# Optimization experiments

Measured on AMD Instinct MI355X. Metric: run time of the kernel, lower is better.

## Reference

```python
import jax, jax.numpy as jnp
import numpy as np
from jax import lax

FEAT_STRIDE = 16
RATIOS = (0.5, 1.0, 2.0)
SCALES = (8.0, 16.0, 32.0)
N_ANCHOR = len(RATIOS) * len(SCALES)  # 9
PRE_NMS = 6000     # ProposalCreator test-mode n_pre_nms
POST_NMS = 300     # test-mode n_post_nms
NMS_THRESH = 0.7
MIN_SIZE = 16.0


def _anchor_base():
    base = 16.0
    py = px = base / 2.0
    r = np.asarray(RATIOS, np.float64)
    s = np.asarray(SCALES, np.float64)
    h = (base * s[None, :] * np.sqrt(r[:, None])).reshape(-1)
    w = (base * s[None, :] * np.sqrt(1.0 / r[:, None])).reshape(-1)
    return np.stack([py - h / 2, px - w / 2, py + h / 2, px + w / 2], axis=1).astype(np.float32)  # [9,4] (y1,x1,y2,x2)


def _enumerate_anchors(H, W):
    base = _anchor_base()
    sy = np.arange(H, dtype=np.float32) * FEAT_STRIDE
    sx = np.arange(W, dtype=np.float32) * FEAT_STRIDE
    yy, xx = np.meshgrid(sy, sx, indexing='ij')
    shift = np.stack([yy, xx, yy, xx], axis=-1).reshape(-1, 1, 4)  # [H*W,1,4]
    return jnp.asarray((shift + base[None]).reshape(-1, 4))  # [H*W*9, 4]


def _loc2bbox(anchors, loc):
    h = anchors[:, 2] - anchors[:, 0]
    w = anchors[:, 3] - anchors[:, 1]
    cy = anchors[:, 0] + 0.5 * h
    cx = anchors[:, 1] + 0.5 * w
    dy, dx, dh, dw = loc[:, 0], loc[:, 1], loc[:, 2], loc[:, 3]
    ny, nx = dy * h + cy, dx * w + cx
    nh, nw = jnp.exp(dh) * h, jnp.exp(dw) * w
    return jnp.stack([ny - 0.5 * nh, nx - 0.5 * nw, ny + 0.5 * nh, nx + 0.5 * nw], axis=1)


def _iou_one(box, boxes):
    ty1 = jnp.maximum(box[0], boxes[:, 0])
    tx1 = jnp.maximum(box[1], boxes[:, 1])
    ty2 = jnp.minimum(box[2], boxes[:, 2])
    tx2 = jnp.minimum(box[3], boxes[:, 3])
    inter = jnp.clip(ty2 - ty1, 0.0) * jnp.clip(tx2 - tx1, 0.0)
    a1 = (box[2] - box[0]) * (box[3] - box[1])
    a2 = (boxes[:, 2] - boxes[:, 0]) * (boxes[:, 3] - boxes[:, 1])
    return inter / jnp.maximum(a1 + a2 - inter, 1e-9)


def _nms_keep(boxes, valid):
    # boxes are sorted by descending score; greedy suppression, fixed shapes
    n = boxes.shape[0]
    idxs = jnp.arange(n)
    def body(i, keep):
        iou = _iou_one(boxes[i], boxes)
        sup = (iou > NMS_THRESH) & (idxs > i)
        return jnp.where(keep[i], keep & ~sup, keep)
    return lax.fori_loop(0, n, body, valid)


def _propose_one(loc, fg, anchors, img_h, img_w, scale):
    boxes = _loc2bbox(anchors, loc)
    boxes = jnp.stack([jnp.clip(boxes[:, 0], 0.0, img_h), jnp.clip(boxes[:, 1], 0.0, img_w),
                       jnp.clip(boxes[:, 2], 0.0, img_h), jnp.clip(boxes[:, 3], 0.0, img_w)], axis=1)
    min_sz = MIN_SIZE * scale
    hs = boxes[:, 2] - boxes[:, 0]
    ws = boxes[:, 3] - boxes[:, 1]
    ok = (hs >= min_sz) & (ws >= min_sz)
    sc = jnp.where(ok, fg, -jnp.inf)
    top_sc, top_idx = lax.top_k(sc, PRE_NMS)
    b = boxes[top_idx]
    keep = _nms_keep(b, jnp.isfinite(top_sc))
    # stable-compact kept boxes to the front, pad to POST_NMS with zeros
    order = jnp.argsort(jnp.where(keep, jnp.arange(PRE_NMS), PRE_NMS))
    sel = order[:POST_NMS]
    n_keep = jnp.sum(keep)
    mask = (jnp.arange(POST_NMS) < n_keep)[:, None].astype(b.dtype)
    return b[sel] * mask  # [POST_NMS, 4], zero-padded


def setup_inputs() -> dict:
    key = jax.random.key(0)
    ks = jax.random.split(key, 5)
    B, C, H, W = 16, 512, 50, 50
    x = jax.random.normal(ks[0], (B, C, H, W), jnp.float32)
    conv1_w = 0.01 * jax.random.normal(ks[1], (512, 512, 3, 3), jnp.float32)
    conv1_b = jnp.zeros((512,), jnp.float32)
    score_w = 0.01 * jax.random.normal(ks[2], (N_ANCHOR * 2, 512, 1, 1), jnp.float32)
    score_b = jnp.zeros((N_ANCHOR * 2,), jnp.float32)
    loc_w = 0.01 * jax.random.normal(ks[3], (N_ANCHOR * 4, 512, 1, 1), jnp.float32)
    loc_b = jnp.zeros((N_ANCHOR * 4,), jnp.float32)
    return {"x": x, "img_h": 800, "img_w": 800,
            "conv1_w": conv1_w, "conv1_b": conv1_b,
            "score_w": score_w, "score_b": score_b,
            "loc_w": loc_w, "loc_b": loc_b}


def reference(x, img_h, img_w, conv1_w, conv1_b, score_w, score_b, loc_w, loc_b):
    B, C, H, W = x.shape
    anchors = _enumerate_anchors(H, W)
    # Faithful to the source bug: `mid = self.conv1(x); mid = relu(x)` -> conv1 output is discarded.
    mid = jax.nn.relu(x)
    # 1x1 convs as einsum; permute(0,2,3,1) + view == bhwo layout then reshape
    locs = jnp.einsum('bchw,oc->bhwo', mid, loc_w[:, :, 0, 0]) + loc_b      # [B,H,W,4A]
    locs = locs.reshape(B, -1, 4)                                            # [B, H*W*A, 4]
    scores_raw = jnp.einsum('bchw,oc->bhwo', mid, score_w[:, :, 0, 0]) + score_b  # [B,H,W,2A]
    sm = jax.nn.softmax(scores_raw.reshape(B, H, W, N_ANCHOR, 2), axis=4)
    fg = sm[..., 1].reshape(B, -1)                                           # [B, H*W*A]
    scores = scores_raw.reshape(B, -1, 2)
    ih = jnp.float32(img_h)
    iw = jnp.float32(img_w)
    rois_b = jax.vmap(lambda l, f: _propose_one(l, f, anchors, ih, iw, 1.0))(locs, fg)  # [B,POST,4]
    rois = rois_b.reshape(-1, 4)
    roi_ix = jnp.repeat(jnp.arange(B, dtype=jnp.int32), POST_NMS)
    return locs, scores, rois, roi_ix, anchors
```

## Files before the change

kernel.cpp:

```cpp
#include <hip/hip_runtime.h>
#include <math.h>

#define NB 16
#define PP 2500
#define WWD 50
#define NANCH 22500
#define CIN 512
#define PRE 6000
#define POST 300
#define NW64 94
#define NW32 188
#define NSEG 16
#define SEG 1408
#define SEGP 2048
#define RUN 6016
#define NMST 512

#define OFF_LOCS   0
#define OFF_SCORES 1440000
#define OFF_ROIS   2160000
#define OFF_ROIIX  2179200
#define OFF_ANCH   2184000

typedef unsigned long long u64;
typedef unsigned u32;

__device__ __forceinline__ void g2l16(const float* g, float* l) {
    __builtin_amdgcn_global_load_lds(
        (const __attribute__((address_space(1))) void*)g,
        (__attribute__((address_space(3))) void*)l, 16, 0, 0);
}

__device__ inline float4 anchor_of(int r) {
    int p = r / 9, a = r - p * 9;
    int gy = p / WWD, gx = p - gy * WWD;
    int ri = a / 3, si = a - ri * 3;
    double ratio = (ri == 0) ? 0.5 : (ri == 1 ? 1.0 : 2.0);
    double scale = (si == 0) ? 8.0 : (si == 1 ? 16.0 : 32.0);
    double hh = 16.0 * scale * sqrt(ratio);
    double wd = 16.0 * scale * sqrt(1.0 / ratio);
    float by1 = (float)(8.0 - hh * 0.5);
    float bx1 = (float)(8.0 - wd * 0.5);
    float by2 = (float)(8.0 + hh * 0.5);
    float bx2 = (float)(8.0 + wd * 0.5);
    float sy = (float)gy * 16.0f, sx = (float)gx * 16.0f;
    return make_float4(sy + by1, sx + bx1, sy + by2, sx + bx2);
}

__device__ inline float4 decode_box(const float* __restrict__ lp, float4 an,
                                    float ih, float iw, bool* ok) {
    float dy = lp[0], dx = lp[1], dh = lp[2], dw = lp[3];
    float h = an.z - an.x, w = an.w - an.y;
    float cy = an.x + 0.5f * h, cx = an.y + 0.5f * w;
    float ny = dy * h + cy, nx = dx * w + cx;
    float nh = expf(dh) * h, nw = expf(dw) * w;
    float y1 = fminf(fmaxf(ny - 0.5f * nh, 0.f), ih);
    float x1 = fminf(fmaxf(nx - 0.5f * nw, 0.f), iw);
    float y2 = fminf(fmaxf(ny + 0.5f * nh, 0.f), ih);
    float x2 = fminf(fmaxf(nx + 0.5f * nw, 0.f), iw);
    *ok = ((y2 - y1) >= 16.0f) && ((x2 - x1) >= 16.0f);
    return make_float4(y1, x1, y2, x2);
}

__device__ inline float iou_f32(float4 a, float4 b) {
    float ty1 = fmaxf(a.x, b.x), tx1 = fmaxf(a.y, b.y);
    float ty2 = fminf(a.z, b.z), tx2 = fminf(a.w, b.w);
    float inter = fmaxf(ty2 - ty1, 0.f) * fmaxf(tx2 - tx1, 0.f);
    float aa = (a.z - a.x) * (a.w - a.y);
    float ab = (b.z - b.x) * (b.w - b.y);
    return inter / fmaxf(aa + ab - inter, 1e-9f);
}

__global__ __launch_bounds__(256) void k_gemm(
    const float* __restrict__ x, const float* __restrict__ lw, const float* __restrict__ lb,
    const float* __restrict__ sw, const float* __restrict__ sb, float* __restrict__ out)
{
    __shared__ __align__(16) float wsL[2][64][16];
    __shared__ __align__(16) float xsL[2][16][64];
    int bid = blockIdx.x;
    int b   = bid / 40;
    int pt  = bid % 40;
    int tid = threadIdx.x;
    int po  = tid & 63;
    int wv  = tid >> 6;
    int og  = __builtin_amdgcn_readfirstlane(wv);
    int ptbase = pt * 64;
    int p0  = ptbase + po;
    bool act0 = (p0 < PP);

    int o0  = og * 14;
    int cnt = (og == 3) ? 12 : 14;
    float bias[14];
#pragma unroll
    for (int k = 0; k < 14; ++k) {
        int o = o0 + k;
        int oc = (o < 54) ? o : 53;
        bias[k] = (oc < 36) ? lb[oc] : sb[oc - 36];
    }

    const float* xrow = x + (size_t)b * (CIN * PP);

    float acc0[14];
#pragma unroll
    for (int k = 0; k < 14; ++k) acc0[k] = 0.f;

    auto stage_async = [&](int buf, int c0) {
        {
            int fbase = og * 256 + po * 4;
            int cc = fbase >> 6;
            int xj = fbase & 63;
            int gpos = ptbase + xj;
            if (gpos > PP - 4) gpos = PP - 4;
            const float* gsrc = xrow + (size_t)(c0 + cc) * PP + gpos;
            float* ldst = &xsL[buf][0][0] + og * 256;
            g2l16(gsrc, ldst);
        }
        {
            int fl = og * 256 + po * 4;
            int o = fl >> 4;
            int c4 = fl & 15;
            const float* gw = (o < 36) ? (lw + (size_t)o * CIN + c0 + c4)
                            : (o < 54) ? (sw + (size_t)(o - 36) * CIN + c0 + c4)
                                       : (lw + c4);
            float* wdst = &wsL[buf][0][0] + og * 256;
            g2l16(gw, wdst);
        }
    };

    stage_async(0, 0);
    __syncthreads();

#pragma unroll 1
    for (int t = 0; t < 32; ++t) {
        int cur = t & 1;
        if (t + 1 < 32) stage_async(cur ^ 1, (t + 1) * 16);
#pragma unroll
        for (int g = 0; g < 4; ++g) {
            float x0[4];
#pragma unroll
            for (int u = 0; u < 4; ++u)
                x0[u] = fmaxf(xsL[cur][g * 4 + u][po], 0.f);
#pragma unroll
            for (int k = 0; k < 14; ++k) {
                float4 w4 = *reinterpret_cast<const float4*>(&wsL[cur][o0 + k][g * 4]);
                acc0[k] += x0[0] * w4.x;
                acc0[k] += x0[1] * w4.y;
                acc0[k] += x0[2] * w4.z;
                acc0[k] += x0[3] * w4.w;
            }
        }
        __syncthreads();
    }

    if (!act0) return;
#pragma unroll
    for (int k = 0; k < 14; ++k) {
        if (k < cnt) {
            int o = o0 + k;
            if (o < 36)
                out[(size_t)OFF_LOCS + ((size_t)b * PP + p0) * 36 + o] = acc0[k] + bias[k];
            else
                out[(size_t)OFF_SCORES + ((size_t)b * PP + p0) * 18 + (o - 36)] = acc0[k] + bias[k];
        }
    }
}

__global__ __launch_bounds__(1024) void k_sort1(
    const float* __restrict__ out_ro, float* __restrict__ out, u64* __restrict__ runs,
    const int* __restrict__ imh_p, const int* __restrict__ imw_p)
{
    __shared__ u64 sk[SEGP];
    int blk = blockIdx.x;
    int b = blk >> 4, s = blk & 15;
    int tid = threadIdx.x;
    int base = s * SEG;
    float ih = (float)imh_p[0], iw = (float)imw_p[0];

    for (int i = tid; i < SEGP; i += 1024) {
        int r = base + i;
        u64 key = 0ull;
        if (i < SEG && r < NANCH) {
            float4 an = anchor_of(r);
            if (b == 0) ((float4*)(out + OFF_ANCH))[r] = an;
            bool ok;
            (void)decode_box(out_ro + (size_t)OFF_LOCS + ((size_t)b * NANCH + r) * 4,
                             an, ih, iw, &ok);
            int p = r / 9, a = r - p * 9;
            const float* sp = out_ro + (size_t)OFF_SCORES + ((size_t)b * PP + p) * 18 + a * 2;
            float s0 = sp[0], s1 = sp[1];
            float mx = fmaxf(s0, s1);
            float e0 = expf(s0 - mx), e1 = expf(s1 - mx);
            float fg = e1 / (e0 + e1);
            float sc = ok ? fg : -INFINITY;
            u32 sb = __float_as_uint(sc);
            sb = (sb & 0x80000000u) ? ~sb : (sb | 0x80000000u);
            key = ((u64)sb << 32) | (u64)(u32)(NANCH - r);
        }
        sk[i] = key;
    }
    __syncthreads();
    for (int kk = 2; kk <= SEGP; kk <<= 1) {
        for (int j = kk >> 1; j > 0; j >>= 1) {
            for (int i = tid; i < SEGP; i += 1024) {
                int ij = i ^ j;
                if (ij > i) {
                    u64 va = sk[i], vb = sk[ij];
                    bool up = ((i & kk) == 0);
                    if (up ? (va < vb) : (va > vb)) { sk[i] = vb; sk[ij] = va; }
                }
            }
            __syncthreads();
        }
    }
    u64* dst = runs + (size_t)blk * SEGP;
    for (int i = tid; i < SEGP; i += 1024) dst[i] = sk[i];
}

__device__ inline int mp_search(const u64* __restrict__ A, const u64* __restrict__ B,
                                int LA, int LB, int d) {
    int lo = max(0, d - LB), hi = min(d, LA);
    while (lo < hi) {
        int mid = (lo + hi) >> 1;
        if (A[mid] > B[d - 1 - mid]) lo = mid + 1; else hi = mid;
    }
    return lo;
}

__global__ __launch_bounds__(1024) void k_merge(
    const u64* __restrict__ in, u64* __restrict__ outk,
    int runLen, int pairsPerBatch, int outLen)
{
    int blk = blockIdx.x;
    int b = blk / pairsPerBatch, m = blk - b * pairsPerBatch;
    const u64* A = in + ((size_t)b * pairsPerBatch * 2 + 2 * m) * runLen;
    const u64* B = A + runLen;
    u64* C = outk + ((size_t)b * pairsPerBatch + m) * outLen;
    int E = (outLen + 1023) >> 10;
    int d0 = threadIdx.x * E;
    if (d0 >= outLen) return;
    int cnt = min(E, outLen - d0);
    int i = mp_search(A, B, runLen, runLen, d0);
    int j = d0 - i;
    for (int e = 0; e < cnt; ++e) {
        u64 va = (i < runLen) ? A[i] : 0ull;
        u64 vb = (j < runLen) ? B[j] : 0ull;
        bool takeA = (j >= runLen) || ((i < runLen) && (va > vb));
        C[d0 + e] = takeA ? va : vb;
        if (takeA) ++i; else ++j;
    }
}

__global__ __launch_bounds__(1024) void k_merge_emit(
    const u64* __restrict__ in, const float* __restrict__ out_ro,
    float* __restrict__ topBoxes, u32* __restrict__ topValid,
    const int* __restrict__ imh_p, const int* __restrict__ imw_p)
{
    int b = blockIdx.x;
    const u64* A = in + (size_t)b * 2 * RUN;
    const u64* B = A + RUN;
    float ih = (float)imh_p[0], iw = (float)imw_p[0];
    int E = (PRE + 1023) >> 10;
    int d0 = threadIdx.x * E;
    if (d0 >= PRE) return;
    int cnt = min(E, PRE - d0);
    int i = mp_search(A, B, RUN, RUN, d0);
    int j = d0 - i;
    for (int e = 0; e < cnt; ++e) {
        u64 va = (i < RUN) ? A[i] : 0ull;
        u64 vb = (j < RUN) ? B[j] : 0ull;
        bool takeA = (j >= RUN) || ((i < RUN) && (va > vb));
        u64 key = takeA ? va : vb;
        if (takeA) ++i; else ++j;
        int d = d0 + e;
        bool valid = (key >> 63) != 0ull;
        int idx = valid ? (NANCH - (int)(key & 0xFFFFFFFFull)) : 0;
        bool ok;
        float4 an = anchor_of(idx);
        float4 bx = decode_box(out_ro + (size_t)OFF_LOCS + ((size_t)b * NANCH + idx) * 4,
                               an, ih, iw, &ok);
        ((float4*)topBoxes)[(size_t)b * PRE + d] = bx;
        topValid[(size_t)b * PRE + d] = valid ? 1u : 0u;
    }
}

__global__ __launch_bounds__(NMST) void k_nms(const float* __restrict__ topBoxes,
                                              const u32* __restrict__ topValid,
                                              float* __restrict__ out)
{
    __shared__ float4 chunkB[64];
    __shared__ float4 keptB[POST];
    __shared__ u32 sup[NW32];
    __shared__ int s_nk;
    __shared__ int s_stop;
    int b = blockIdx.x, tid = threadIdx.x;
    int wave = tid >> 6, lane = tid & 63;
    const float4* tb = (const float4*)topBoxes + (size_t)b * PRE;

    for (int i = tid; i < NW32; i += NMST) sup[i] = 0u;
    if (tid == 0) { s_nk = 0; s_stop = 0; }
    __syncthreads();
    for (int r = tid; r < PRE; r += NMST)
        if (!topValid[(size_t)b * PRE + r]) atomicOr(&sup[r >> 5], 1u << (r & 31));
    if (tid == 0) atomicOr(&sup[187], 0xFFFF0000u);
    __syncthreads();

    for (int c = 0; c < NW64; ++c) {
        int base = c * 64;
        if (tid < 64)
            chunkB[tid] = (base + tid < PRE) ? tb[base + tid]
                                             : make_float4(0.f, 0.f, 0.f, 0.f);
        int nk0 = s_nk;
        bool s = false;
        if (nk0 > 0 && base + lane < PRE) {
            float4 bj = tb[base + lane];
            for (int t = wave; t < nk0; t += 8)
                s |= iou_f32(keptB[t], bj) > 0.7f;
        }
        u64 bal = __ballot(s);
        if (lane == 0 && bal) {
            atomicOr(&sup[2 * c], (u32)bal);
            atomicOr(&sup[2 * c + 1], (u32)(bal >> 32));
        }
        __syncthreads();
        if (wave == 0) {
            u64 avail = ~(((u64)sup[2 * c + 1] << 32) | (u64)sup[2 * c]);
            float4 myB = chunkB[lane];
            int nkl = s_nk;
            while (avail && nkl < POST) {
                int i = __builtin_ctzll(avail);
                float4 bi = chunkB[i];
                if (lane == 0) keptB[nkl] = bi;
                nkl++;
                bool ss = iou_f32(bi, myB) > 0.7f;
                u64 bb = __ballot(ss);
                avail &= ~((1ull << i) | bb);
            }
            if (lane == 0) { s_nk = nkl; if (nkl >= POST) s_stop = 1; }
        }
        __syncthreads();
        if (s_stop) break;
    }

    __syncthreads();
    int nk = min(s_nk, POST);
    for (int r = tid; r < POST; r += NMST) {
        float4 v = make_float4(0.f, 0.f, 0.f, 0.f);
        if (r < nk) v = keptB[r];
        ((float4*)(out + OFF_ROIS))[(size_t)b * POST + r] = v;
        out[(size_t)OFF_ROIIX + (size_t)b * POST + r] = (float)b;
    }
}

extern "C" void kernel_launch(void* const* d_in, const int* in_sizes, int n_in,
                              void* d_out, int out_size, void* d_ws, size_t ws_size,
                              hipStream_t stream) {
    const float* x  = (const float*)d_in[0];
    const int* imh  = (const int*)d_in[1];
    const int* imw  = (const int*)d_in[2];
    const float* sw = (const float*)d_in[5];
    const float* sb = (const float*)d_in[6];
    const float* lw = (const float*)d_in[7];
    const float* lb = (const float*)d_in[8];
    float* out = (float*)d_out;
    char* wsb = (char*)d_ws;

    u64*   runs0    = (u64*)(wsb);
    u64*   runs1    = (u64*)(wsb + 4194304);
    u64*   runs2    = (u64*)(wsb + 8388608);
    u64*   runs3    = (u64*)(wsb + 11468800);
    float* topBoxes = (float*)(wsb + 13008896);
    u32*   topValid = (u32*)(wsb + 14544896);

    hipLaunchKernelGGL(k_gemm, dim3(NB * 40), dim3(256), 0, stream,
                       x, lw, lb, sw, sb, out);
    hipLaunchKernelGGL(k_sort1, dim3(NB * NSEG), dim3(1024), 0, stream,
                       out, out, runs0, imh, imw);
    hipLaunchKernelGGL(k_merge, dim3(NB * 8), dim3(1024), 0, stream,
                       runs0, runs1, SEGP, 8, 4096);
    hipLaunchKernelGGL(k_merge, dim3(NB * 4), dim3(1024), 0, stream,
                       runs1, runs2, 4096, 4, RUN);
    hipLaunchKernelGGL(k_merge, dim3(NB * 2), dim3(1024), 0, stream,
                       runs2, runs3, RUN, 2, RUN);
    hipLaunchKernelGGL(k_merge_emit, dim3(NB), dim3(1024), 0, stream,
                       runs3, out, topBoxes, topValid, imh, imw);
    hipLaunchKernelGGL(k_nms, dim3(NB), dim3(NMST), 0, stream,
                       topBoxes, topValid, out);
}
```

Baseline: 239.8 us.

## Fuse merge passes into two kernels with shared-memory intermediate runs

Replaces the four merge-path kernel launches with two. Each new kernel does two merge levels, keeping the first level's output in LDS instead of writing it to global memory. This removes two launches and two global round trips of the intermediate sorted runs. In exchange it uses 64 KB and 96 KB of shared memory per block, which cuts occupancy, and the final merge runs on only 16 blocks.

```diff
diff --git a/kernel.cpp b/kernel.cpp
--- a/kernel.cpp
+++ b/kernel.cpp
@@ -216,8 +216,7 @@
     for (int i = tid; i < SEGP; i += 1024) dst[i] = sk[i];
 }
 
-__device__ inline int mp_search(const u64* __restrict__ A, const u64* __restrict__ B,
-                                int LA, int LB, int d) {
+__device__ inline int mp_search(const u64* A, const u64* B, int LA, int LB, int d) {
     int lo = max(0, d - LB), hi = min(d, LA);
     while (lo < hi) {
         int mid = (lo + hi) >> 1;
@@ -226,48 +225,68 @@
     return lo;
 }
 
-__global__ __launch_bounds__(1024) void k_merge(
-    const u64* __restrict__ in, u64* __restrict__ outk,
-    int runLen, int pairsPerBatch, int outLen)
-{
-    int blk = blockIdx.x;
-    int b = blk / pairsPerBatch, m = blk - b * pairsPerBatch;
-    const u64* A = in + ((size_t)b * pairsPerBatch * 2 + 2 * m) * runLen;
-    const u64* B = A + runLen;
-    u64* C = outk + ((size_t)b * pairsPerBatch + m) * outLen;
-    int E = (outLen + 1023) >> 10;
-    int d0 = threadIdx.x * E;
-    if (d0 >= outLen) return;
-    int cnt = min(E, outLen - d0);
-    int i = mp_search(A, B, runLen, runLen, d0);
+__device__ inline void mp_merge_seg(const u64* A, const u64* B, int LA, int LB,
+                                    int d0, int cnt, u64* dst) {
+    int i = mp_search(A, B, LA, LB, d0);
     int j = d0 - i;
     for (int e = 0; e < cnt; ++e) {
-        u64 va = (i < runLen) ? A[i] : 0ull;
-        u64 vb = (j < runLen) ? B[j] : 0ull;
-        bool takeA = (j >= runLen) || ((i < runLen) && (va > vb));
-        C[d0 + e] = takeA ? va : vb;
+        u64 va = (i < LA) ? A[i] : 0ull;
+        u64 vb = (j < LB) ? B[j] : 0ull;
+        bool takeA = (j >= LB) || ((i < LA) && (va > vb));
+        dst[d0 + e] = takeA ? va : vb;
         if (takeA) ++i; else ++j;
     }
 }
 
-__global__ __launch_bounds__(1024) void k_merge_emit(
+__global__ __launch_bounds__(1024) void k_mergeA(
+    const u64* __restrict__ in, u64* __restrict__ outk)
+{
+    __shared__ u64 bufA[4096];
+    __shared__ u64 bufB[4096];
+    int blk = blockIdx.x;
+    int b = blk >> 2, m = blk & 3;
+    int tid = threadIdx.x;
+    const u64* s0 = in + ((size_t)b * NSEG + 4 * m) * SEGP;
+    const u64* s1 = s0 + SEGP;
+    const u64* s2 = s1 + SEGP;
+    const u64* s3 = s2 + SEGP;
+    mp_merge_seg(s0, s1, SEGP, SEGP, tid * 4, 4, bufA);
+    mp_merge_seg(s2, s3, SEGP, SEGP, tid * 4, 4, bufB);
+    __syncthreads();
+    int d0 = tid * 6;
+    if (d0 < RUN)
+        mp_merge_seg(bufA, bufB, 4096, 4096, d0, min(6, RUN - d0),
+                     outk + ((size_t)b * 4 + m) * RUN);
+}
+
+__global__ __launch_bounds__(1024) void k_mergeB_emit(
     const u64* __restrict__ in, const float* __restrict__ out_ro,
     float* __restrict__ topBoxes, u32* __restrict__ topValid,
     const int* __restrict__ imh_p, const int* __restrict__ imw_p)
 {
+    __shared__ u64 bufA[RUN];
+    __shared__ u64 bufB[RUN];
     int b = blockIdx.x;
-    const u64* A = in + (size_t)b * 2 * RUN;
-    const u64* B = A + RUN;
+    int tid = threadIdx.x;
+    const u64* r0 = in + (size_t)b * 4 * RUN;
+    const u64* r1 = r0 + RUN;
+    const u64* r2 = r1 + RUN;
+    const u64* r3 = r2 + RUN;
+    int d0 = tid * 6;
+    if (d0 < RUN) {
+        int c = min(6, RUN - d0);
+        mp_merge_seg(r0, r1, RUN, RUN, d0, c, bufA);
+        mp_merge_seg(r2, r3, RUN, RUN, d0, c, bufB);
+    }
+    __syncthreads();
     float ih = (float)imh_p[0], iw = (float)imw_p[0];
-    int E = (PRE + 1023) >> 10;
-    int d0 = threadIdx.x * E;
     if (d0 >= PRE) return;
-    int cnt = min(E, PRE - d0);
-    int i = mp_search(A, B, RUN, RUN, d0);
+    int cnt = min(6, PRE - d0);
+    int i = mp_search(bufA, bufB, RUN, RUN, d0);
     int j = d0 - i;
     for (int e = 0; e < cnt; ++e) {
-        u64 va = (i < RUN) ? A[i] : 0ull;
-        u64 vb = (j < RUN) ? B[j] : 0ull;
+        u64 va = (i < RUN) ? bufA[i] : 0ull;
+        u64 vb = (j < RUN) ? bufB[j] : 0ull;
         bool takeA = (j >= RUN) || ((i < RUN) && (va > vb));
         u64 key = takeA ? va : vb;
         if (takeA) ++i; else ++j;
@@ -366,23 +385,17 @@
 
     u64*   runs0    = (u64*)(wsb);
     u64*   runs1    = (u64*)(wsb + 4194304);
-    u64*   runs2    = (u64*)(wsb + 8388608);
-    u64*   runs3    = (u64*)(wsb + 11468800);
-    float* topBoxes = (float*)(wsb + 13008896);
-    u32*   topValid = (u32*)(wsb + 14544896);
+    float* topBoxes = (float*)(wsb + 7274496);
+    u32*   topValid = (u32*)(wsb + 8810496);
 
     hipLaunchKernelGGL(k_gemm, dim3(NB * 40), dim3(256), 0, stream,
                        x, lw, lb, sw, sb, out);
     hipLaunchKernelGGL(k_sort1, dim3(NB * NSEG), dim3(1024), 0, stream,
                        out, out, runs0, imh, imw);
-    hipLaunchKernelGGL(k_merge, dim3(NB * 8), dim3(1024), 0, stream,
-                       runs0, runs1, SEGP, 8, 4096);
-    hipLaunchKernelGGL(k_merge, dim3(NB * 4), dim3(1024), 0, stream,
-                       runs1, runs2, 4096, 4, RUN);
-    hipLaunchKernelGGL(k_merge, dim3(NB * 2), dim3(1024), 0, stream,
-                       runs2, runs3, RUN, 2, RUN);
-    hipLaunchKernelGGL(k_merge_emit, dim3(NB), dim3(1024), 0, stream,
-                       runs3, out, topBoxes, topValid, imh, imw);
+    hipLaunchKernelGGL(k_mergeA, dim3(NB * 4), dim3(1024), 0, stream,
+                       runs0, runs1);
+    hipLaunchKernelGGL(k_mergeB_emit, dim3(NB), dim3(1024), 0, stream,
+                       runs1, out, topBoxes, topValid, imh, imw);
     hipLaunchKernelGGL(k_nms, dim3(NB), dim3(NMST), 0, stream,
                        topBoxes, topValid, out);
 }
```

Result: faster. 232.7 us, median of 2 (-3.0%).
